# Performance work log

Hardware: AMD Instinct MI355X
Metric: run time of the kernel (lower is better)

## Reference

```python
import jax, jax.numpy as jnp
import numpy as np


def setup_inputs() -> dict:
    key = jax.random.key(0)
    k1, k2, k3 = jax.random.split(key, 3)
    dim, heads, dim_head, rows = 512, 8, 64, 64
    b, t = 4, 256
    _dim = heads * dim_head
    x = jax.random.normal(k1, (b * rows, t, dim), dtype=jnp.float32)
    # torch nn.Linear weight layout: [out_features, in_features]
    W_qkv = jax.random.normal(k2, (3 * _dim, dim), dtype=jnp.float32) * (dim ** -0.5)
    W0 = jax.random.normal(k3, (dim, _dim), dtype=jnp.float32) * (_dim ** -0.5)
    return {"x": x, "W_qkv": W_qkv, "W0": W0, "rows": rows, "heads": heads}


def reference(x, W_qkv, W0, rows, heads):
    br, t, dim = x.shape
    b = br // rows
    three_dim = W_qkv.shape[0]
    dim_head = three_dim // (3 * heads)
    scale = (rows * dim_head) ** -0.5

    qkv = x @ W_qkv.T  # [(b*rows), t, 3*heads*dim_head]
    # einops '(b rows) t (d k h) -> k b rows h t d': last dim ordered (d, k, h)
    qkv = qkv.reshape(b, rows, t, dim_head, 3, heads)
    qkv = jnp.transpose(qkv, (4, 0, 1, 5, 2, 3))  # [3, b, rows, h, t, d]
    q, k, v = qkv[0], qkv[1], qkv[2]

    # tied-row attention: sum QK^T over rows before a single shared softmax
    scores = jnp.einsum('brhid,brhjd->bhij', q, k) * scale  # [b, h, t, t]
    attn = jax.nn.softmax(scores, axis=-1)
    # broadcast shared attention map back across rows
    out = jnp.einsum('bhij,brhjd->brhid', attn, v)  # [b, rows, h, t, d]
    # 'b rows h t d -> (b rows) t (h d)'
    out = jnp.transpose(out, (0, 1, 3, 2, 4)).reshape(br, t, heads * dim_head)
    return out @ W0.T
```

## Files before the change

kernel.cpp:

```cpp
#include <hip/hip_runtime.h>


typedef short  bf16x8 __attribute__((ext_vector_type(8)));
typedef float  f32x4  __attribute__((ext_vector_type(4)));

#define MFMA16(a,b,c) __builtin_amdgcn_mfma_f32_16x16x32_bf16((a),(b),(c),0,0,0)

__device__ __forceinline__ ushort f2bf(float f) {
  union { float f; unsigned u; } v; v.f = f;
  unsigned r = v.u + 0x7fffu + ((v.u >> 16) & 1u);
  return (ushort)(r >> 16);
}

__device__ __forceinline__ void gload_lds16(const void* g, void* lds) {
  __builtin_amdgcn_global_load_lds(
      (const __attribute__((address_space(1))) void*)g,
      (__attribute__((address_space(3))) void*)lds, 16, 0, 0);
}


__global__ void cast_f32_to_bf16(const float* __restrict__ in,
                                 ushort* __restrict__ out, int n4) {
  int idx = blockIdx.x * blockDim.x + threadIdx.x;
  int stride = gridDim.x * blockDim.x;
  for (int v = idx; v < n4; v += stride) {
    float4 f = reinterpret_cast<const float4*>(in)[v];
    ushort4 o; o.x = f2bf(f.x); o.y = f2bf(f.y); o.z = f2bf(f.z); o.w = f2bf(f.w);
    reinterpret_cast<ushort4*>(out)[v] = o;
  }
}

__global__ void prep_k(const float* __restrict__ W, ushort* __restrict__ Wp,
                       const float* __restrict__ W0, ushort* __restrict__ W0b) {
  const int bid = blockIdx.x, tid = threadIdx.x;
  if (bid < 768) {
    int np = (bid << 1) + (tid >> 7);
    int c  = tid & 127;
    int k = np >> 9, h = (np >> 6) & 7, d = np & 63;
    float4 f = reinterpret_cast<const float4*>(
        W + (size_t)(d * 24 + k * 8 + h) * 512)[c];
    ushort4 u; u.x = f2bf(f.x); u.y = f2bf(f.y); u.z = f2bf(f.z); u.w = f2bf(f.w);
    reinterpret_cast<ushort4*>(Wp + (size_t)np * 512)[c] = u;
  } else {
    int v0 = ((bid - 768) << 10) + (tid << 2);
#pragma unroll
    for (int q = 0; q < 4; ++q) {
      int v = v0 + q;
      float4 f = reinterpret_cast<const float4*>(W0)[v];
      ushort4 u; u.x = f2bf(f.x); u.y = f2bf(f.y); u.z = f2bf(f.z); u.w = f2bf(f.w);
      reinterpret_cast<ushort4*>(W0b)[v] = u;
    }
  }
}


__device__ __forceinline__ void gemm_nt_256x128(
    const ushort* __restrict__ A, const ushort* __restrict__ B,
    int lda, int ldb, int P, int m0, int n0, char* lds, f32x4 (&acc)[8][4]) {
  const int tid = threadIdx.x;
  const int w = tid >> 6, l = tid & 63;
  const int il = l & 15, kl = l >> 4;
  const int wm = w >> 1, wn = w & 1;

  auto stageA = [&](char* buf, int kt) {
#pragma unroll
    for (int c = 0; c < 4; ++c) {
      int rbase = (w << 6) + (c << 4);
      int row = rbase + (l >> 2);
      int s = ((l & 3) - ((row >> 1) & 3)) & 3;
      gload_lds16(A + (size_t)(m0 + row) * lda + (kt << 5) + (s << 3),
                  buf + rbase * 64);
    }
  };
  auto stageB = [&](char* buf, int kt) {
#pragma unroll
    for (int c = 0; c < 2; ++c) {
      int rbase = (w << 5) + (c << 4);
      int row = rbase + (l >> 2);
      int s = ((l & 3) - ((row >> 1) & 3)) & 3;
      gload_lds16(B + (size_t)(n0 + row) * ldb + (kt << 5) + (s << 3),
                  buf + 16384 + rbase * 64);
    }
  };
  auto loadA8 = [&](const char* buf, bf16x8 (&af)[8]) {
#pragma unroll
    for (int q = 0; q < 8; ++q) {
      int row = (wm << 7) + (q << 4) + il;
      af[q] = *(const bf16x8*)(buf + row * 64 + (((kl + (row >> 1)) & 3) << 4));
    }
  };
  auto loadB4 = [&](const char* buf, bf16x8 (&bfr)[4]) {
#pragma unroll
    for (int q = 0; q < 4; ++q) {
      int row = (wn << 6) + (q << 4) + il;
      bfr[q] = *(const bf16x8*)(buf + 16384 + row * 64 + (((kl + (row >> 1)) & 3) << 4));
    }
  };

#pragma unroll
  for (int i = 0; i < 8; ++i)
#pragma unroll
    for (int j = 0; j < 4; ++j) acc[i][j] = f32x4{0.f, 0.f, 0.f, 0.f};

  stageA(lds, 0);         stageB(lds, 0);
  stageA(lds + 24576, 1); stageB(lds + 24576, 1);
  asm volatile("s_waitcnt vmcnt(6)" ::: "memory");
  __builtin_amdgcn_s_barrier();

  int cur = 0, nx = 2;
  for (int g = 0; g < P; ++g) {
    char* cbuf = lds + cur * 24576;
    char* sbuf = lds + nx * 24576;
    bf16x8 af[8], bfr[4];
    loadA8(cbuf, af);
    loadB4(cbuf, bfr);
    if (g + 2 < P) { stageA(sbuf, g + 2); stageB(sbuf, g + 2); }
    __builtin_amdgcn_s_setprio(1);
#pragma unroll
    for (int fm = 0; fm < 8; ++fm)
#pragma unroll
      for (int fn = 0; fn < 4; ++fn)
        acc[fm][fn] = MFMA16(af[fm], bfr[fn], acc[fm][fn]);
    __builtin_amdgcn_s_setprio(0);
    if (g + 2 < P) asm volatile("s_waitcnt vmcnt(6)" ::: "memory");
    else           asm volatile("s_waitcnt vmcnt(0)" ::: "memory");
    __builtin_amdgcn_s_barrier();
    cur = (cur == 2) ? 0 : cur + 1;
    nx  = (nx  == 2) ? 0 : nx  + 1;
  }
}


__global__ __launch_bounds__(256, 2) void gemm_qkv_k(
    const ushort* __restrict__ xb, const ushort* __restrict__ Wp,
    ushort* __restrict__ Qb, ushort* __restrict__ Kb, ushort* __restrict__ Vt) {
  __shared__ __align__(16) char lds[73728];
  f32x4 acc[8][4];
  const int Bid = blockIdx.x;
  const int xcd = Bid & 7, idx = Bid >> 3;
  const int nt = idx % 12, pl = idx / 12;
  const int m0 = ((pl << 3) + xcd) << 8;
  const int n0 = nt << 7;
  gemm_nt_256x128(xb, Wp, 512, 512, 16, m0, n0, lds, acc);

  const int tid = threadIdx.x, w = tid >> 6, l = tid & 63;
  const int il = l & 15, kl = l >> 4;
  const int wm = w >> 1, wn = w & 1;
  const int kq = n0 >> 9;
  const int br = m0 >> 8, b = br >> 6, r = br & 63;

  if (kq < 2) {
    ushort* Pl = (ushort*)lds;
    __syncthreads();
#pragma unroll
    for (int fm = 0; fm < 8; ++fm)
#pragma unroll
      for (int fn = 0; fn < 4; ++fn) {
        int ccol = (wn << 6) + (fn << 4) + il;
#pragma unroll
        for (int j = 0; j < 4; ++j) {
          int irow = (wm << 7) + (fm << 4) + (kl << 2) + j;
          Pl[irow * 136 + ccol] = f2bf(acc[fm][fn][j]);
        }
      }
    __syncthreads();
    ushort* dstb = kq ? Kb : Qb;
#pragma unroll
    for (int it = 0; it < 16; ++it) {
      int u = (it << 8) + tid;
      int row = u >> 4, n8 = (u & 15);
      int n_full = n0 + (n8 << 3);
      int h = (n_full >> 6) & 7, d0 = n_full & 63;
      bf16x8 v = *(const bf16x8*)(Pl + row * 136 + (n8 << 3));
      size_t dst = ((size_t)((((b << 3) + h) << 8) + row) << 12) + (r << 6) + d0;
      *reinterpret_cast<bf16x8*>(&dstb[dst]) = v;
    }
  } else {
#pragma unroll
    for (int fm = 0; fm < 8; ++fm)
#pragma unroll
      for (int fn = 0; fn < 4; ++fn) {
        int n = n0 - 1024 + (wn << 6) + (fn << 4) + il;
        int h = n >> 6, d = n & 63;
        int i0 = (wm << 7) + (fm << 4) + (kl << 2);
        size_t dst = (((size_t)((((b << 3) + h) << 12)) + (r << 6) + d) << 8) + i0;
        ushort4 pk; pk.x = f2bf(acc[fm][fn][0]); pk.y = f2bf(acc[fm][fn][1]);
        pk.z = f2bf(acc[fm][fn][2]); pk.w = f2bf(acc[fm][fn][3]);
        *reinterpret_cast<ushort4*>(&Vt[dst]) = pk;
      }
  }
}


__global__ __launch_bounds__(256, 2) void gemm_out_k(
    const ushort* __restrict__ O2, const ushort* __restrict__ W0b,
    float* __restrict__ out) {
  __shared__ __align__(16) char lds[73728];
  f32x4 acc[8][4];
  const int Bid = blockIdx.x;
  const int xcd = Bid & 7, idx = Bid >> 3;
  const int nt = idx & 3, pl = idx >> 2;
  const int m0 = ((pl << 3) + xcd) << 8;
  const int n0 = nt << 7;
  gemm_nt_256x128(O2, W0b, 512, 512, 16, m0, n0, lds, acc);

  const int tid = threadIdx.x, w = tid >> 6, l = tid & 63;
  const int il = l & 15, kl = l >> 4;
  const int wm = w >> 1, wn = w & 1;
#pragma unroll
  for (int fm = 0; fm < 8; ++fm)
#pragma unroll
    for (int fn = 0; fn < 4; ++fn) {
      int n = n0 + (wn << 6) + (fn << 4) + il;
#pragma unroll
      for (int j = 0; j < 4; ++j) {
        int m = m0 + (wm << 7) + (fm << 4) + (kl << 2) + j;
        out[(size_t)m * 512 + n] = acc[fm][fn][j];
      }
    }
}


__global__ __launch_bounds__(256, 2) void gemm_s_k(
    const ushort* __restrict__ Qb, const ushort* __restrict__ Kb,
    float* __restrict__ Sp) {
  __shared__ __align__(16) char lds[73728];
  f32x4 acc[8][4];
  const int Bid = blockIdx.x;
  const int nt = Bid & 1, z = Bid >> 1;
  const int bh = z >> 2, ks = z & 3;
  const int n0 = nt << 7;
  const size_t base = ((size_t)bh << 20) + ((size_t)ks << 10);
  gemm_nt_256x128(Qb + base, Kb + base, 4096, 4096, 32, 0, n0, lds, acc);

  const int tid = threadIdx.x, w = tid >> 6, l = tid & 63;
  const int il = l & 15, kl = l >> 4;
  const int wm = w >> 1, wn = w & 1;
  float* o = Sp + ((size_t)z << 16);
#pragma unroll
  for (int fm = 0; fm < 8; ++fm)
#pragma unroll
    for (int fn = 0; fn < 4; ++fn) {
      int n = n0 + (wn << 6) + (fn << 4) + il;
#pragma unroll
      for (int j = 0; j < 4; ++j) {
        int m = (wm << 7) + (fm << 4) + (kl << 2) + j;
        o[(size_t)m * 256 + n] = acc[fm][fn][j];
      }
    }
}


__global__ void softmax_k(const float* __restrict__ Sp, ushort* __restrict__ Pb) {
  const int w = threadIdx.x >> 6, l = threadIdx.x & 63;
  const int row = (blockIdx.x << 2) + w;
  const int bh = row >> 8, i = row & 255;
  const float4* p0 = reinterpret_cast<const float4*>(
      Sp + (((size_t)bh << 2) << 16) + ((size_t)i << 8)) + l;
  float4 a = p0[0], b2 = p0[16384], c = p0[32768], d = p0[49152];
  const float scale = 0.015625f;
  float s0 = (a.x + b2.x + c.x + d.x) * scale;
  float s1 = (a.y + b2.y + c.y + d.y) * scale;
  float s2 = (a.z + b2.z + c.z + d.z) * scale;
  float s3 = (a.w + b2.w + c.w + d.w) * scale;
  float m = fmaxf(fmaxf(s0, s1), fmaxf(s2, s3));
#pragma unroll
  for (int d2 = 1; d2 < 64; d2 <<= 1) m = fmaxf(m, __shfl_xor(m, d2));
  float e0 = __expf(s0 - m), e1 = __expf(s1 - m);
  float e2 = __expf(s2 - m), e3 = __expf(s3 - m);
  float sum = e0 + e1 + e2 + e3;
#pragma unroll
  for (int d2 = 1; d2 < 64; d2 <<= 1) sum += __shfl_xor(sum, d2);
  float r = 1.0f / sum;
  ushort4 p; p.x = f2bf(e0 * r); p.y = f2bf(e1 * r);
  p.z = f2bf(e2 * r); p.w = f2bf(e3 * r);
  reinterpret_cast<ushort4*>(Pb + ((size_t)bh << 16) + ((size_t)i << 8))[l] = p;
}


__global__ __launch_bounds__(256, 2) void gemm_pv_k(
    const ushort* __restrict__ Vt, const ushort* __restrict__ Pb,
    ushort* __restrict__ O2) {
  __shared__ __align__(16) char lds[73728];
  f32x4 acc[8][4];
  const int Bid = blockIdx.x;
  const int xcd = Bid & 7, idx = Bid >> 3;
  const int sub = idx & 31, grp = idx >> 5;
  const int bh = (grp << 3) + xcd, b = bh >> 3, h = bh & 7;
  const int m0 = (sub >> 1) << 8;
  const int n0 = (sub & 1) << 7;
  gemm_nt_256x128(Vt + ((size_t)bh << 20), Pb + ((size_t)bh << 16),
                  256, 256, 8, m0, n0, lds, acc);

  const int tid = threadIdx.x, w = tid >> 6, l = tid & 63;
  const int il = l & 15, kl = l >> 4;
  const int wm = w >> 1, wn = w & 1;
#pragma unroll
  for (int fm = 0; fm < 8; ++fm) {
    int rd0 = m0 + (wm << 7) + (fm << 4) + (kl << 2);
    int r = rd0 >> 6, d0 = rd0 & 63;
#pragma unroll
    for (int fn = 0; fn < 4; ++fn) {
      int i = n0 + (wn << 6) + (fn << 4) + il;
      ushort4 pk; pk.x = f2bf(acc[fm][fn][0]); pk.y = f2bf(acc[fm][fn][1]);
      pk.z = f2bf(acc[fm][fn][2]); pk.w = f2bf(acc[fm][fn][3]);
      *reinterpret_cast<ushort4*>(
          O2 + ((size_t)((((b << 6) + r) << 8) + i) << 9) + (h << 6) + d0) = pk;
    }
  }
}


extern "C" void kernel_launch(void* const* d_in, const int* in_sizes, int n_in,
                              void* d_out, int out_size, void* d_ws, size_t ws_size,
                              hipStream_t stream) {
  const float* x    = (const float*)d_in[0];
  const float* Wqkv = (const float*)d_in[1];
  const float* W0   = (const float*)d_in[2];
  float* out = (float*)d_out;

  char* ws = (char*)d_ws;
  ushort* xb  = (ushort*)(ws);
  ushort* Wp  = (ushort*)(ws + 67108864);
  ushort* W0b = (ushort*)(ws + 68681728);
  ushort* Qb  = (ushort*)(ws + 69206016);
  ushort* Kb  = (ushort*)(ws + 136314880);
  ushort* Vt  = (ushort*)(ws + 203423744);
  if (ws_size < 270532608ull) return;

  cast_f32_to_bf16<<<2048, 256, 0, stream>>>(x, xb, 8388608);
  prep_k<<<832, 256, 0, stream>>>(Wqkv, Wp, W0, W0b);

  gemm_qkv_k<<<3072, 256, 0, stream>>>(xb, Wp, Qb, Kb, Vt);

  float*  Sp = (float*)xb;
  ushort* Pb = Qb;
  ushort* O2 = xb;

  gemm_s_k<<<256, 256, 0, stream>>>(Qb, Kb, Sp);
  softmax_k<<<2048, 256, 0, stream>>>(Sp, Pb);
  gemm_pv_k<<<1024, 256, 0, stream>>>(Vt, Pb, O2);

  gemm_out_k<<<1024, 256, 0, stream>>>(O2, W0b, out);
}
```

Measured before the change: 309.8 us.

## Merge prep kernels, store bf16 partial scores, remap S grid, drop LDS epilogue

Folds the x cast and the weight prep into one launch. Partial QK^T scores are now stored as bf16 instead of fp32, halving the score traffic between gemm_s_k and softmax_k. gemm_s_k blocks are reordered so each XCD handles whole heads. The Q/K epilogue of the QKV GEMM now writes scalar bf16 values straight to global memory instead of staging through LDS for 16-byte stores, which removes two barriers but may give poorly coalesced writes; the bf16 partial sums also lose some precision.

```diff
diff --git a/kernel.cpp b/kernel.cpp
--- a/kernel.cpp
+++ b/kernel.cpp
@@ -12,6 +12,11 @@
   return (ushort)(r >> 16);
 }
 
+__device__ __forceinline__ float bf2f(ushort u) {
+  union { unsigned u; float f; } v; v.u = ((unsigned)u) << 16;
+  return v.f;
+}
+
 __device__ __forceinline__ void gload_lds16(const void* g, void* lds) {
   __builtin_amdgcn_global_load_lds(
       (const __attribute__((address_space(1))) void*)g,
@@ -19,22 +24,21 @@
 }
 
 
-__global__ void cast_f32_to_bf16(const float* __restrict__ in,
-                                 ushort* __restrict__ out, int n4) {
-  int idx = blockIdx.x * blockDim.x + threadIdx.x;
-  int stride = gridDim.x * blockDim.x;
-  for (int v = idx; v < n4; v += stride) {
-    float4 f = reinterpret_cast<const float4*>(in)[v];
-    ushort4 o; o.x = f2bf(f.x); o.y = f2bf(f.y); o.z = f2bf(f.z); o.w = f2bf(f.w);
-    reinterpret_cast<ushort4*>(out)[v] = o;
-  }
-}
-
-__global__ void prep_k(const float* __restrict__ W, ushort* __restrict__ Wp,
-                       const float* __restrict__ W0, ushort* __restrict__ W0b) {
+__global__ void prep_all_k(const float* __restrict__ x, ushort* __restrict__ xb,
+                           const float* __restrict__ W, ushort* __restrict__ Wp,
+                           const float* __restrict__ W0, ushort* __restrict__ W0b) {
   const int bid = blockIdx.x, tid = threadIdx.x;
-  if (bid < 768) {
-    int np = (bid << 1) + (tid >> 7);
+  if (bid < 2048) {
+    int v0 = (bid << 12) + tid;
+#pragma unroll
+    for (int q = 0; q < 16; ++q) {
+      int v = v0 + (q << 8);
+      float4 f = reinterpret_cast<const float4*>(x)[v];
+      ushort4 u; u.x = f2bf(f.x); u.y = f2bf(f.y); u.z = f2bf(f.z); u.w = f2bf(f.w);
+      reinterpret_cast<ushort4*>(xb)[v] = u;
+    }
+  } else if (bid < 2816) {
+    int np = ((bid - 2048) << 1) + (tid >> 7);
     int c  = tid & 127;
     int k = np >> 9, h = (np >> 6) & 7, d = np & 63;
     float4 f = reinterpret_cast<const float4*>(
@@ -42,7 +46,7 @@
     ushort4 u; u.x = f2bf(f.x); u.y = f2bf(f.y); u.z = f2bf(f.z); u.w = f2bf(f.w);
     reinterpret_cast<ushort4*>(Wp + (size_t)np * 512)[c] = u;
   } else {
-    int v0 = ((bid - 768) << 10) + (tid << 2);
+    int v0 = ((bid - 2816) << 10) + (tid << 2);
 #pragma unroll
     for (int q = 0; q < 4; ++q) {
       int v = v0 + q;
@@ -150,31 +154,20 @@
   const int br = m0 >> 8, b = br >> 6, r = br & 63;
 
   if (kq < 2) {
-    ushort* Pl = (ushort*)lds;
-    __syncthreads();
+    ushort* dstb = kq ? Kb : Qb;
 #pragma unroll
     for (int fm = 0; fm < 8; ++fm)
 #pragma unroll
       for (int fn = 0; fn < 4; ++fn) {
-        int ccol = (wn << 6) + (fn << 4) + il;
+        int n = n0 + (wn << 6) + (fn << 4) + il;
+        int h = (n >> 6) & 7, d = n & 63;
 #pragma unroll
         for (int j = 0; j < 4; ++j) {
-          int irow = (wm << 7) + (fm << 4) + (kl << 2) + j;
-          Pl[irow * 136 + ccol] = f2bf(acc[fm][fn][j]);
+          int i = (wm << 7) + (fm << 4) + (kl << 2) + j;
+          size_t dst = ((size_t)((((b << 3) + h) << 8) + i) << 12) + (r << 6) + d;
+          dstb[dst] = f2bf(acc[fm][fn][j]);
         }
       }
-    __syncthreads();
-    ushort* dstb = kq ? Kb : Qb;
-#pragma unroll
-    for (int it = 0; it < 16; ++it) {
-      int u = (it << 8) + tid;
-      int row = u >> 4, n8 = (u & 15);
-      int n_full = n0 + (n8 << 3);
-      int h = (n_full >> 6) & 7, d0 = n_full & 63;
-      bf16x8 v = *(const bf16x8*)(Pl + row * 136 + (n8 << 3));
-      size_t dst = ((size_t)((((b << 3) + h) << 8) + row) << 12) + (r << 6) + d0;
-      *reinterpret_cast<bf16x8*>(&dstb[dst]) = v;
-    }
   } else {
 #pragma unroll
     for (int fm = 0; fm < 8; ++fm)
@@ -223,12 +216,14 @@
 
 __global__ __launch_bounds__(256, 2) void gemm_s_k(
     const ushort* __restrict__ Qb, const ushort* __restrict__ Kb,
-    float* __restrict__ Sp) {
+    ushort* __restrict__ Spb) {
   __shared__ __align__(16) char lds[73728];
   f32x4 acc[8][4];
   const int Bid = blockIdx.x;
-  const int nt = Bid & 1, z = Bid >> 1;
-  const int bh = z >> 2, ks = z & 3;
+  const int xcd = Bid & 7, t = Bid >> 3;
+  const int j8 = t & 7, bh = ((t >> 3) << 3) + xcd;
+  const int ks = j8 >> 1, nt = j8 & 1;
+  const int z = (bh << 2) + ks;
   const int n0 = nt << 7;
   const size_t base = ((size_t)bh << 20) + ((size_t)ks << 10);
   gemm_nt_256x128(Qb + base, Kb + base, 4096, 4096, 32, 0, n0, lds, acc);
@@ -236,7 +231,7 @@
   const int tid = threadIdx.x, w = tid >> 6, l = tid & 63;
   const int il = l & 15, kl = l >> 4;
   const int wm = w >> 1, wn = w & 1;
-  float* o = Sp + ((size_t)z << 16);
+  ushort* o = Spb + ((size_t)z << 16);
 #pragma unroll
   for (int fm = 0; fm < 8; ++fm)
 #pragma unroll
@@ -245,24 +240,26 @@
 #pragma unroll
       for (int j = 0; j < 4; ++j) {
         int m = (wm << 7) + (fm << 4) + (kl << 2) + j;
-        o[(size_t)m * 256 + n] = acc[fm][fn][j];
+        o[(size_t)m * 256 + n] = f2bf(acc[fm][fn][j]);
       }
     }
 }
 
 
-__global__ void softmax_k(const float* __restrict__ Sp, ushort* __restrict__ Pb) {
+__global__ void softmax_k(const ushort* __restrict__ Spb, ushort* __restrict__ Pb) {
   const int w = threadIdx.x >> 6, l = threadIdx.x & 63;
   const int row = (blockIdx.x << 2) + w;
   const int bh = row >> 8, i = row & 255;
-  const float4* p0 = reinterpret_cast<const float4*>(
-      Sp + (((size_t)bh << 2) << 16) + ((size_t)i << 8)) + l;
-  float4 a = p0[0], b2 = p0[16384], c = p0[32768], d = p0[49152];
+  const ushort4* p0 = reinterpret_cast<const ushort4*>(
+      Spb + (((size_t)bh << 2) << 16) + ((size_t)i << 8)) + l;
+  float s0 = 0.f, s1 = 0.f, s2 = 0.f, s3 = 0.f;
+#pragma unroll
+  for (int ks = 0; ks < 4; ++ks) {
+    ushort4 a = p0[(size_t)ks * 16384];
+    s0 += bf2f(a.x); s1 += bf2f(a.y); s2 += bf2f(a.z); s3 += bf2f(a.w);
+  }
   const float scale = 0.015625f;
-  float s0 = (a.x + b2.x + c.x + d.x) * scale;
-  float s1 = (a.y + b2.y + c.y + d.y) * scale;
-  float s2 = (a.z + b2.z + c.z + d.z) * scale;
-  float s3 = (a.w + b2.w + c.w + d.w) * scale;
+  s0 *= scale; s1 *= scale; s2 *= scale; s3 *= scale;
   float m = fmaxf(fmaxf(s0, s1), fmaxf(s2, s3));
 #pragma unroll
   for (int d2 = 1; d2 < 64; d2 <<= 1) m = fmaxf(m, __shfl_xor(m, d2));
@@ -328,17 +325,16 @@
   ushort* Vt  = (ushort*)(ws + 203423744);
   if (ws_size < 270532608ull) return;
 
-  cast_f32_to_bf16<<<2048, 256, 0, stream>>>(x, xb, 8388608);
-  prep_k<<<832, 256, 0, stream>>>(Wqkv, Wp, W0, W0b);
+  prep_all_k<<<2880, 256, 0, stream>>>(x, xb, Wqkv, Wp, W0, W0b);
 
   gemm_qkv_k<<<3072, 256, 0, stream>>>(xb, Wp, Qb, Kb, Vt);
 
-  float*  Sp = (float*)xb;
-  ushort* Pb = Qb;
-  ushort* O2 = xb;
-
-  gemm_s_k<<<256, 256, 0, stream>>>(Qb, Kb, Sp);
-  softmax_k<<<2048, 256, 0, stream>>>(Sp, Pb);
+  ushort* Spb = xb;
+  ushort* Pb  = Qb;
+  ushort* O2  = xb;
+
+  gemm_s_k<<<256, 256, 0, stream>>>(Qb, Kb, Spb);
+  softmax_k<<<2048, 256, 0, stream>>>(Spb, Pb);
   gemm_pv_k<<<1024, 256, 0, stream>>>(Vt, Pb, O2);
 
   gemm_out_k<<<1024, 256, 0, stream>>>(O2, W0b, out);
```

New measurement: 289.3 us. -6.6%, faster.
